# Optimization experiments

Hardware: AMD Instinct MI355X
Metric: run time of the kernel (lower is better)

## Reference

```python
import jax, jax.numpy as jnp
import numpy as np

N = 100000   # nodes (rows of origin_data, and unique values in edge_index)
E = 2000000  # edges
CIN = 16     # conv input channels
T = 8        # time dim of origin_data
HUMAN_EXHALATION_FLOW = 0.0001 * 40000  # = 4.0


def setup_inputs() -> dict:
    key = jax.random.key(0)
    k1, k2, k3, k4, k5, k6 = jax.random.split(key, 6)
    # keep size (origin_data[:, -1, 2]) away from zero since it is a divisor
    origin_data = jax.random.uniform(k1, (N, T, 3), jnp.float32) + 0.1
    x = jax.random.normal(k2, (E, 1, CIN), jnp.float32)
    # edge_index must contain every node id 0..N-1 (node_list = zeros_like(edge_index.unique()))
    src = jnp.concatenate([jnp.arange(N, dtype=jnp.int32),
                           jax.random.randint(k3, (E - N,), 0, N, dtype=jnp.int32)])
    dst = jax.random.randint(k4, (E,), 0, N, dtype=jnp.int32)
    edge_index = jnp.stack([src, dst])  # [2, E]
    conv_w = jax.random.normal(k5, (1, CIN, 1, 1), jnp.float32) * 0.1  # [out, in, kh, kw]
    conv_b = jax.random.normal(k6, (1,), jnp.float32) * 0.1
    return {"origin_data": origin_data, "x": x, "conv_w": conv_w,
            "conv_b": conv_b, "edge_index": edge_index}


def reference(origin_data, x, conv_w, conv_b, edge_index):
    concentration = origin_data[:, -1, 0]  # [N]
    people = origin_data[:, -1, 1]         # [N]
    size = origin_data[:, -1, 2]           # [N]

    # 1x1 conv over [1, CIN, E, 1] == per-edge linear: [E,1,CIN] -> [E,1,1]
    out = jnp.einsum('ewc,oc->ewo', x, conv_w[:, :, 0, 0]) + conv_b
    flow = out  # [E,1,1]

    # torch loop uses .item() everywhere -> values are detached constants
    val = jax.lax.stop_gradient(out[:, 0, 0])        # [E]
    conc_d = jax.lax.stop_gradient(concentration)
    size_d = jax.lax.stop_gradient(size)

    src, dst = edge_index[0], edge_index[1]
    valid = src != dst  # self-loops skipped
    # per edge i: write node_list_new[src] = val*conc[src]/size[src] (order 2i)
    #             then node_list_new[dst] = val*conc[src]/size[dst] (order 2i+1)
    v_src = val * conc_d[src] / size_d[src]
    v_dst = val * conc_d[src] / size_d[dst]
    ar = jnp.arange(E, dtype=jnp.int32)
    ids = jnp.concatenate([src, dst])                       # [2E]
    vals = jnp.concatenate([v_src, v_dst])                  # [2E]
    orders = jnp.concatenate([jnp.where(valid, 2 * ar, -1),
                              jnp.where(valid, 2 * ar + 1, -1)])
    max_ord = jax.ops.segment_max(orders, ids, num_segments=N)  # last valid write per node
    sel = (orders >= 0) & (orders == max_ord[ids])              # unique winner per node
    node_list_new = jnp.zeros(N, dtype=val.dtype).at[ids].add(jnp.where(sel, vals, 0.0))

    exhaled = jax.lax.stop_gradient(HUMAN_EXHALATION_FLOW * people / size_d)  # .item() detaches
    result = concentration + node_list_new + exhaled
    return result[:, None], flow
```

## Files before the change

### kernel.cpp

```cpp
#include <hip/hip_runtime.h>

#define N_NODES 100000
#define E_EDGES 2000000
#define SPLIT_E 1800000
#define CIN 16
#define EXH_FLOW 4.0f


__global__ void init_nodes_kernel(const float* __restrict__ origin,
                                  float* __restrict__ out,
                                  int* __restrict__ max_ord,
                                  float* __restrict__ conc_c,
                                  float* __restrict__ rsize_c,
                                  unsigned char* __restrict__ settled) {
    int n = blockIdx.x * blockDim.x + threadIdx.x;
    if (n >= N_NODES) return;
    size_t base = (size_t)n * 24;
    float conc   = origin[base + 21];
    float people = origin[base + 22];
    float size   = origin[base + 23];
    float rs = 1.0f / size;
    out[n] = conc + EXH_FLOW * people * rs;
    conc_c[n]  = conc;
    rsize_c[n] = rs;
    max_ord[n] = -1;
    settled[n] = 0;
}

__global__ void scatter_top_kernel(const int* __restrict__ src,
                                   const int* __restrict__ dst,
                                   int* __restrict__ max_ord,
                                   unsigned char* __restrict__ settled) {
    int i = blockIdx.x * blockDim.x + threadIdx.x;
    int e = SPLIT_E + i;
    if (e >= E_EDGES) return;
    int s = src[e], d = dst[e];
    if (s != d) {
        atomicMax(&max_ord[s], 2 * e);
        atomicMax(&max_ord[d], 2 * e + 1);
        settled[s] = 1;
        settled[d] = 1;
    }
}

__global__ void fused_flow_scatter_kernel(const float4* __restrict__ xv,
                                          const float* __restrict__ w,
                                          const float* __restrict__ b,
                                          const int* __restrict__ src,
                                          const int* __restrict__ dst,
                                          const unsigned char* __restrict__ settled,
                                          float* __restrict__ flow,
                                          int* __restrict__ max_ord) {
    int tid = blockIdx.x * blockDim.x + threadIdx.x;
    if (tid >= E_EDGES * 4) return;
    int q = tid & 3;
    int e = tid >> 2;
    float4 v  = xv[tid];
    float4 wq = ((const float4*)w)[q];
    float p = v.x * wq.x + v.y * wq.y + v.z * wq.z + v.w * wq.w;
    p += __shfl_xor(p, 1);
    p += __shfl_xor(p, 2);
    if (q == 0) {
        flow[e] = p + b[0];
        int s = src[e], d = dst[e];
        if (s != d) {
            if (!settled[s]) atomicMax(&max_ord[s], 2 * e);
            if (!settled[d]) atomicMax(&max_ord[d], 2 * e + 1);
        }
    }
}

__global__ void finalize_kernel(const int* __restrict__ src,
                                const float* __restrict__ flow,
                                const int* __restrict__ max_ord,
                                const float* __restrict__ conc_c,
                                const float* __restrict__ rsize_c,
                                float* __restrict__ out) {
    int n = blockIdx.x * blockDim.x + threadIdx.x;
    if (n >= N_NODES) return;
    int o = max_ord[n];
    if (o < 0) return;
    int e = o >> 1;
    float val = flow[e];
    float v;
    if ((o & 1) == 0) {
        v = val * conc_c[n] * rsize_c[n];
    } else {
        int s = src[e];
        v = val * conc_c[s] * rsize_c[n];
    }
    out[n] += v;
}

extern "C" void kernel_launch(void* const* d_in, const int* in_sizes, int n_in,
                              void* d_out, int out_size, void* d_ws, size_t ws_size,
                              hipStream_t stream) {
    const float* origin = (const float*)d_in[0];
    const float* x      = (const float*)d_in[1];
    const float* conv_w = (const float*)d_in[2];
    const float* conv_b = (const float*)d_in[3];
    const int*   eidx   = (const int*)d_in[4];
    const int* src = eidx;
    const int* dst = eidx + E_EDGES;

    float* out  = (float*)d_out;
    float* flow = out + N_NODES;

    int*           max_ord = (int*)d_ws;
    float*         conc_c  = (float*)((char*)d_ws + 1 * 400 * 1024);
    float*         rsize_c = (float*)((char*)d_ws + 2 * 400 * 1024);
    unsigned char* settled = (unsigned char*)((char*)d_ws + 3 * 400 * 1024);

    const int BLK = 256;
    init_nodes_kernel<<<(N_NODES + BLK - 1) / BLK, BLK, 0, stream>>>(
        origin, out, max_ord, conc_c, rsize_c, settled);
    scatter_top_kernel<<<((E_EDGES - SPLIT_E) + BLK - 1) / BLK, BLK, 0, stream>>>(
        src, dst, max_ord, settled);
    fused_flow_scatter_kernel<<<((E_EDGES * 4) + BLK - 1) / BLK, BLK, 0, stream>>>(
        (const float4*)x, conv_w, conv_b, src, dst, settled, flow, max_ord);
    finalize_kernel<<<(N_NODES + BLK - 1) / BLK, BLK, 0, stream>>>(
        src, flow, max_ord, conc_c, rsize_c, out);
}
```

Measured before the change: 65.95 us.

## Split flow GEMV and scatter into separate block roles with vectorized edge loads

The fused kernel had every fourth lane do the scatter work, which left most lanes idle and diverged during the atomic section. Now the kernel is one launch whose blocks take one of two roles. Some blocks compute the per-edge conv flow using all lanes. The other blocks each process 8 edges per thread, loading src and dst as int4 and issuing the settled-filtered atomicMax updates. This decouples the memory-bound x stream from the latency-bound atomics, at the cost of more atomics in flight per thread.

```diff
diff --git a/kernel.cpp b/kernel.cpp
--- a/kernel.cpp
+++ b/kernel.cpp
@@ -5,6 +5,14 @@
 #define SPLIT_E 1800000
 #define CIN 16
 #define EXH_FLOW 4.0f
+#define TOP_E (E_EDGES - SPLIT_E)
+
+#define BLK 256
+#define FLOW_THREADS (E_EDGES * 4)
+#define FLOW_BLOCKS  (FLOW_THREADS / BLK)
+#define SCAT_EPT 8
+#define SCAT_THREADS (SPLIT_E / SCAT_EPT)
+#define SCAT_BLOCKS  ((SCAT_THREADS + BLK - 1) / BLK)
 
 
 __global__ void init_nodes_kernel(const float* __restrict__ origin,
@@ -43,30 +51,45 @@
     }
 }
 
-__global__ void fused_flow_scatter_kernel(const float4* __restrict__ xv,
-                                          const float* __restrict__ w,
-                                          const float* __restrict__ b,
-                                          const int* __restrict__ src,
-                                          const int* __restrict__ dst,
-                                          const unsigned char* __restrict__ settled,
-                                          float* __restrict__ flow,
-                                          int* __restrict__ max_ord) {
-    int tid = blockIdx.x * blockDim.x + threadIdx.x;
-    if (tid >= E_EDGES * 4) return;
-    int q = tid & 3;
-    int e = tid >> 2;
-    float4 v  = xv[tid];
-    float4 wq = ((const float4*)w)[q];
-    float p = v.x * wq.x + v.y * wq.y + v.z * wq.z + v.w * wq.w;
-    p += __shfl_xor(p, 1);
-    p += __shfl_xor(p, 2);
-    if (q == 0) {
-        flow[e] = p + b[0];
-        int s = src[e], d = dst[e];
-        if (s != d) {
-            if (!settled[s]) atomicMax(&max_ord[s], 2 * e);
-            if (!settled[d]) atomicMax(&max_ord[d], 2 * e + 1);
+__global__ void main_pass_kernel(const float4* __restrict__ xv,
+                                 const float* __restrict__ w,
+                                 const float* __restrict__ b,
+                                 const int* __restrict__ src,
+                                 const int* __restrict__ dst,
+                                 const unsigned char* __restrict__ settled,
+                                 float* __restrict__ flow,
+                                 int* __restrict__ max_ord) {
+    if (blockIdx.x < FLOW_BLOCKS) {
+        int tid = blockIdx.x * BLK + threadIdx.x;
+        int q = tid & 3;
+        float4 v  = xv[tid];
+        float4 wq = ((const float4*)w)[q];
+        float p = v.x * wq.x + v.y * wq.y + v.z * wq.z + v.w * wq.w;
+        p += __shfl_xor(p, 1);
+        p += __shfl_xor(p, 2);
+        if (q == 0) flow[tid >> 2] = p + b[0];
+    } else {
+        int t = (blockIdx.x - FLOW_BLOCKS) * BLK + threadIdx.x;
+        int e0 = t * SCAT_EPT;
+        if (e0 >= SPLIT_E) return;
+        int4 sa = *(const int4*)(src + e0);
+        int4 sb = *(const int4*)(src + e0 + 4);
+        int4 da = *(const int4*)(dst + e0);
+        int4 db = *(const int4*)(dst + e0 + 4);
+#define PROC(EE, SS, DD)                                                  \
+        if ((SS) != (DD)) {                                               \
+            if (!settled[SS]) atomicMax(&max_ord[SS], 2 * (EE));          \
+            if (!settled[DD]) atomicMax(&max_ord[DD], 2 * (EE) + 1);      \
         }
+        PROC(e0 + 0, sa.x, da.x)
+        PROC(e0 + 1, sa.y, da.y)
+        PROC(e0 + 2, sa.z, da.z)
+        PROC(e0 + 3, sa.w, da.w)
+        PROC(e0 + 4, sb.x, db.x)
+        PROC(e0 + 5, sb.y, db.y)
+        PROC(e0 + 6, sb.z, db.z)
+        PROC(e0 + 7, sb.w, db.w)
+#undef PROC
     }
 }
 
@@ -111,12 +134,11 @@
     float*         rsize_c = (float*)((char*)d_ws + 2 * 400 * 1024);
     unsigned char* settled = (unsigned char*)((char*)d_ws + 3 * 400 * 1024);
 
-    const int BLK = 256;
     init_nodes_kernel<<<(N_NODES + BLK - 1) / BLK, BLK, 0, stream>>>(
         origin, out, max_ord, conc_c, rsize_c, settled);
-    scatter_top_kernel<<<((E_EDGES - SPLIT_E) + BLK - 1) / BLK, BLK, 0, stream>>>(
+    scatter_top_kernel<<<(TOP_E + BLK - 1) / BLK, BLK, 0, stream>>>(
         src, dst, max_ord, settled);
-    fused_flow_scatter_kernel<<<((E_EDGES * 4) + BLK - 1) / BLK, BLK, 0, stream>>>(
+    main_pass_kernel<<<FLOW_BLOCKS + SCAT_BLOCKS, BLK, 0, stream>>>(
         (const float4*)x, conv_w, conv_b, src, dst, settled, flow, max_ord);
     finalize_kernel<<<(N_NODES + BLK - 1) / BLK, BLK, 0, stream>>>(
         src, flow, max_ord, conc_c, rsize_c, out);
```

Measured after the change: 82.77 us. 25.5% more time.
